# Performance work log

Hardware: AMD Instinct MI355X
Metric: run time of the kernel (lower is better)

Reference implementation:

```python
import jax, jax.numpy as jnp
import numpy as np

N = 50000          # nodes
E = 1000000        # edges
EMB = 64           # emb_dim
L = 3              # num_layer
B = 250            # graphs (200 nodes each)
XF, EF = 7, 5      # node / edge feature dims
BN_EPS = 1e-5


def setup_inputs() -> dict:
    key = jax.random.key(0)
    ks = jax.random.split(key, 16)
    x = jax.random.normal(ks[0], (N, XF), dtype=jnp.float32)
    edge_attr = jax.random.normal(ks[1], (E, EF), dtype=jnp.float32)
    edge_index = jax.random.randint(ks[2], (2, E), 0, N, dtype=jnp.int32)
    # 250 contiguous graphs of 200 nodes: last node index of each graph
    last_idx = jnp.arange(1, B + 1, dtype=jnp.int32) * (N // B) - 1
    s = 0.05
    xW = jax.random.normal(ks[3], (XF, EMB), dtype=jnp.float32) * s
    xb = jnp.zeros((EMB,), dtype=jnp.float32)
    eW = jax.random.normal(ks[4], (L, EF, EMB), dtype=jnp.float32) * s
    eb = jnp.zeros((L, EMB), dtype=jnp.float32)
    W1 = jax.random.normal(ks[5], (L, EMB, 2 * EMB), dtype=jnp.float32) * s
    b1 = jnp.zeros((L, 2 * EMB), dtype=jnp.float32)
    W2 = jax.random.normal(ks[6], (L, 2 * EMB, EMB), dtype=jnp.float32) * s
    b2 = jnp.zeros((L, EMB), dtype=jnp.float32)
    gamma = jnp.ones((L, EMB), dtype=jnp.float32)
    beta = jnp.zeros((L, EMB), dtype=jnp.float32)
    return {"x": x, "edge_attr": edge_attr, "edge_index": edge_index,
            "last_idx": last_idx, "xW": xW, "xb": xb, "eW": eW, "eb": eb,
            "W1": W1, "b1": b1, "W2": W2, "b2": b2,
            "gamma": gamma, "beta": beta}


def _gnn_forward(x, edge_attr, edge_index, last_idx, xW, xb, eW, eb, W1, b1, W2, b2, gamma, beta):
    n = x.shape[0]
    # self-loop edge attrs: first column = 8, rest 0
    self_attr = jnp.zeros((n, EF), dtype=edge_attr.dtype).at[:, 0].set(8.0)
    ea = jnp.concatenate([edge_attr, self_attr], axis=0)          # [E+N, EF]
    loop = jnp.arange(n, dtype=edge_index.dtype)
    src = jnp.concatenate([edge_index[0], loop])                  # x_j indices
    dst = jnp.concatenate([edge_index[1], loop])                  # aggregation targets

    h = x @ xW + xb                                               # [N, EMB]
    for l in range(L):
        e = ea @ eW[l] + eb[l]                                    # [E+N, EMB]
        msg = h[src] + e                                          # gather + combine
        agg = jax.ops.segment_sum(msg, dst, num_segments=n)       # scatter-add
        h2 = jax.nn.relu(agg @ W1[l] + b1[l]) @ W2[l] + b2[l]     # GIN MLP
        mean = jnp.mean(h2, axis=0)
        var = jnp.mean(jnp.square(h2 - mean), axis=0)             # biased, like torch BN
        hn = (h2 - mean) * jax.lax.rsqrt(var + BN_EPS) * gamma[l] + beta[l]
        h = jax.nn.elu(hn) if l < L - 1 else hn                   # drop_ratio = 0
    return h[last_idx]                                            # super-node reps [B, EMB]


def reference(x, edge_attr, edge_index, last_idx, xW, xb, eW, eb, W1, b1, W2, b2, gamma, beta):
    return _gnn_forward(x, edge_attr, edge_index, last_idx, xW, xb, eW, eb, W1, b1, W2, b2, gamma, beta)
```

## Files before the change

### kernel.cpp

```cpp
#include <hip/hip_runtime.h>

#define N_NODES 50000
#define N_EDGES 1000000
#define EMB     64
#define HID     128
#define NLAYER  3
#define NGRAPH  250
#define XFD     7
#define EFD     5
#define BN_EPS  1e-5f

#define BKT_SH 8
#define BKT_SZ 256
#define NBKT   ((N_NODES + BKT_SZ - 1) / BKT_SZ)
#define CHKE   4096
#define NCHK   ((N_EDGES + CHKE - 1) / CHKE)
#define CNTM   (NBKT * NCHK)
#define NB2    ((CNTM + 255) / 256)

typedef short bf8_t __attribute__((ext_vector_type(8)));
typedef float f4_t  __attribute__((ext_vector_type(4)));

union FragU {
    uint4 q;
    bf8_t v;
    unsigned short u[8];
};

__device__ __forceinline__ void atomAddF(float* p, float v) {
    __hip_atomic_fetch_add(p, v, __ATOMIC_RELAXED, __HIP_MEMORY_SCOPE_AGENT);
}

__device__ __forceinline__ unsigned short f2bf(float f) {
    unsigned int u = __float_as_uint(f);
    u += 0x7fffu + ((u >> 16) & 1u);
    return (unsigned short)(u >> 16);
}
__device__ __forceinline__ float bf2f(unsigned short s) {
    return __uint_as_float(((unsigned int)s) << 16);
}
__device__ __forceinline__ float4 bf4(ushort4 u) {
    return make_float4(bf2f(u.x), bf2f(u.y), bf2f(u.z), bf2f(u.w));
}

__global__ void k_input(const float* __restrict__ x, const float* __restrict__ xW,
                        const float* __restrict__ xb, unsigned short* __restrict__ h) {
    int gid = blockIdx.x * 256 + threadIdx.x;
    if (gid >= N_NODES * EMB) return;
    int n = gid >> 6, f = gid & 63;
    float acc = xb[f];
#pragma unroll
    for (int k = 0; k < XFD; ++k) acc = fmaf(x[n * XFD + k], xW[k * EMB + f], acc);
    h[gid] = f2bf(acc);
}

__global__ void k_packW(const float* __restrict__ W1, const float* __restrict__ W2,
                        unsigned short* __restrict__ pw1, unsigned short* __restrict__ pw2) {
    int gid = blockIdx.x * 256 + threadIdx.x;
    int layer = gid >> 14;
    int r = gid & 16383;
    if (layer >= NLAYER) return;
    if (r < 8192) {
        int p = r;
        int j = p & 7, lane = (p >> 3) & 63, ts = p >> 9;
        int t = ts >> 1, s = ts & 1;
        int k = 32 * s + 8 * (lane >> 4) + j;
        int n = 16 * t + (lane & 15);
        pw1[layer * 8192 + p] = f2bf(W1[layer * EMB * HID + k * HID + n]);
    } else {
        int p = r - 8192;
        int j = p & 7, lane = (p >> 3) & 63, ts = p >> 9;
        int t = ts >> 2, s = ts & 3;
        int k = 32 * s + 8 * (lane >> 4) + j;
        int n = 16 * t + (lane & 15);
        pw2[layer * 8192 + p] = f2bf(W2[layer * HID * EMB + k * EMB + n]);
    }
}

__global__ __launch_bounds__(256) void k_binA(const int* __restrict__ dst,
                                              int* __restrict__ cntmat) {
    __shared__ int hist[NBKT];
    int tid = threadIdx.x, c = blockIdx.x;
    for (int i = tid; i < NBKT; i += 256) hist[i] = 0;
    __syncthreads();
    int e0 = c * CHKE, e1 = min(e0 + CHKE, N_EDGES);
    for (int i = e0 + tid; i < e1; i += 256) atomicAdd(&hist[dst[i] >> BKT_SH], 1);
    __syncthreads();
    for (int b = tid; b < NBKT; b += 256) cntmat[b * NCHK + c] = hist[b];
}

__global__ __launch_bounds__(256) void k_gscanA(const int* __restrict__ in, int n,
                                                int* __restrict__ bsum) {
    int tid = threadIdx.x, lane = tid & 63, wid = tid >> 6;
    int i = blockIdx.x * 256 + tid;
    int v = (i < n) ? in[i] : 0;
#pragma unroll
    for (int off = 32; off; off >>= 1) v += __shfl_down(v, off);
    __shared__ int ws[4];
    if (lane == 0) ws[wid] = v;
    __syncthreads();
    if (tid == 0) bsum[blockIdx.x] = ws[0] + ws[1] + ws[2] + ws[3];
}

__global__ __launch_bounds__(256) void k_gscanB(const int* __restrict__ bsum, int nb,
                                                int* __restrict__ boff) {
    int tid = threadIdx.x, lane = tid & 63, wid = tid >> 6;
    int v = (tid < nb) ? bsum[tid] : 0;
    int x = v;
#pragma unroll
    for (int off = 1; off < 64; off <<= 1) {
        int y = __shfl_up(x, off);
        if (lane >= off) x += y;
    }
    __shared__ int wtot[4];
    if (lane == 63) wtot[wid] = x;
    __syncthreads();
    int woff = 0;
    for (int w = 0; w < wid; ++w) woff += wtot[w];
    if (tid < nb) boff[tid] = woff + x - v;
}

__global__ __launch_bounds__(256) void k_gscanC(const int* __restrict__ in, int n,
                                                const int* __restrict__ boff,
                                                int* __restrict__ out) {
    int tid = threadIdx.x, lane = tid & 63, wid = tid >> 6;
    int i = blockIdx.x * 256 + tid;
    int v = (i < n) ? in[i] : 0;
    int x = v;
#pragma unroll
    for (int off = 1; off < 64; off <<= 1) {
        int y = __shfl_up(x, off);
        if (lane >= off) x += y;
    }
    __shared__ int wtot[4];
    if (lane == 63) wtot[wid] = x;
    __syncthreads();
    int woff = boff[blockIdx.x];
    for (int w = 0; w < wid; ++w) woff += wtot[w];
    if (i < n) out[i] = woff + x - v;
}

__global__ __launch_bounds__(256) void k_binC(const int* __restrict__ src,
                                              const int* __restrict__ dst,
                                              const int* __restrict__ off2,
                                              int2* __restrict__ bufSD) {
    __shared__ int cur[NBKT];
    int tid = threadIdx.x, c = blockIdx.x;
    for (int b = tid; b < NBKT; b += 256) cur[b] = off2[b * NCHK + c];
    __syncthreads();
    int e0 = c * CHKE, e1 = min(e0 + CHKE, N_EDGES);
    for (int i = e0 + tid; i < e1; i += 256) {
        int d = dst[i];
        int b = d >> BKT_SH;
        int p = atomicAdd(&cur[b], 1);
        bufSD[p] = make_int2(src[i], ((d & (BKT_SZ - 1)) << 20) | i);
    }
}

__global__ __launch_bounds__(256) void k_binD(const int2* __restrict__ bufSD,
                                              const int* __restrict__ off2,
                                              int* __restrict__ csr,
                                              int* __restrict__ csrE,
                                              int* __restrict__ rowstart) {
    __shared__ int hist[BKT_SZ];
    __shared__ int cur[BKT_SZ];
    __shared__ int wtot[4];
    int tid = threadIdx.x, b = blockIdx.x;
    int bstart = off2[b * NCHK];
    int bend = (b + 1 < NBKT) ? off2[(b + 1) * NCHK] : N_EDGES;
    hist[tid] = 0;
    __syncthreads();
    for (int j = bstart + tid; j < bend; j += 256)
        atomicAdd(&hist[bufSD[j].y >> 20], 1);
    __syncthreads();
    int lane = tid & 63, wid = tid >> 6;
    int v = hist[tid], x = v;
#pragma unroll
    for (int off = 1; off < 64; off <<= 1) {
        int y = __shfl_up(x, off);
        if (lane >= off) x += y;
    }
    if (lane == 63) wtot[wid] = x;
    __syncthreads();
    int woff = 0;
    for (int w = 0; w < wid; ++w) woff += wtot[w];
    int ex = woff + x - v;
    cur[tid] = ex;
    int node = b * BKT_SZ + tid;
    if (node < N_NODES) rowstart[node] = bstart + ex;
    if (b == NBKT - 1 && tid == 0) rowstart[N_NODES] = N_EDGES;
    __syncthreads();
    for (int j = bstart + tid; j < bend; j += 256) {
        int2 t = bufSD[j];
        int local = t.y >> 20;
        int p = atomicAdd(&cur[local], 1);
        csr[bstart + p] = t.x;
        csrE[bstart + p] = t.y & 0xFFFFF;
    }
}

__global__ __launch_bounds__(256) void k_aggE(const int* __restrict__ rowstart,
                                              const int* __restrict__ csrE,
                                              const float* __restrict__ ea,
                                              float* __restrict__ aggE) {
    int wid = (blockIdx.x * 256 + threadIdx.x) >> 6;
    int lane = threadIdx.x & 63;
    if (wid >= N_NODES) return;
    int j0 = rowstart[wid], j1 = rowstart[wid + 1];
    float s0 = 0.f, s1 = 0.f, s2 = 0.f, s3 = 0.f, s4 = 0.f;
    for (int j = j0 + lane; j < j1; j += 64) {
        int e = csrE[j];
        const float* p = ea + (size_t)e * EFD;
        s0 += p[0]; s1 += p[1]; s2 += p[2]; s3 += p[3]; s4 += p[4];
    }
#pragma unroll
    for (int off = 32; off; off >>= 1) {
        s0 += __shfl_down(s0, off);
        s1 += __shfl_down(s1, off);
        s2 += __shfl_down(s2, off);
        s3 += __shfl_down(s3, off);
        s4 += __shfl_down(s4, off);
    }
    if (lane == 0) {
        float* o = aggE + (size_t)wid * EFD;
        o[0] = s0; o[1] = s1; o[2] = s2; o[3] = s3; o[4] = s4;
    }
}

__global__ __launch_bounds__(256) void k_agg(const unsigned short* __restrict__ h,
                                             float* __restrict__ agg,
                                             const int* __restrict__ rowstart,
                                             const int* __restrict__ csr,
                                             const float* __restrict__ aggE,
                                             const float* __restrict__ eWl,
                                             const float* __restrict__ ebl) {
    int wave = (blockIdx.x * 256 + threadIdx.x) >> 6;
    int lane = threadIdx.x & 63;
    int nbase = wave * 4;
    if (nbase >= N_NODES) return;
    int lg = lane >> 4, lq = lane & 15;
    const ushort4* hb = (const ushort4*)h;
    const float4* eW4 = (const float4*)eWl;
    float4 ew0 = eW4[lq], ew1 = eW4[16 + lq], ew2 = eW4[32 + lq],
           ew3 = eW4[48 + lq], ew4 = eW4[64 + lq];
    float4 eb4 = ((const float4*)ebl)[lq];
    int nend = min(nbase + 4, N_NODES);
    for (int n = nbase; n < nend; ++n) {
        int j0 = rowstart[n], j1 = rowstart[n + 1];
        float4 acc = make_float4(0.f, 0.f, 0.f, 0.f);
        int j = j0;
        while (j < j1) {
            int take = j1 - j;
            if (take > 64) take = 64;
            int myid = (lane < take) ? csr[j + lane] : 0;
            int nt = (take + 3) >> 2;
            int t = 0;
            for (; t + 4 <= nt; t += 4) {
                int e0 = t * 4 + lg, e1 = e0 + 4, e2 = e0 + 8, e3 = e0 + 12;
                int s0 = __shfl(myid, e0), s1 = __shfl(myid, e1),
                    s2 = __shfl(myid, e2), s3 = __shfl(myid, e3);
                float4 v0 = bf4(hb[(size_t)s0 * 16 + lq]);
                float4 v1 = bf4(hb[(size_t)s1 * 16 + lq]);
                float4 v2 = bf4(hb[(size_t)s2 * 16 + lq]);
                float4 v3 = bf4(hb[(size_t)s3 * 16 + lq]);
                if (e0 < take) { acc.x += v0.x; acc.y += v0.y; acc.z += v0.z; acc.w += v0.w; }
                if (e1 < take) { acc.x += v1.x; acc.y += v1.y; acc.z += v1.z; acc.w += v1.w; }
                if (e2 < take) { acc.x += v2.x; acc.y += v2.y; acc.z += v2.z; acc.w += v2.w; }
                if (e3 < take) { acc.x += v3.x; acc.y += v3.y; acc.z += v3.z; acc.w += v3.w; }
            }
            for (; t < nt; ++t) {
                int e = t * 4 + lg;
                int s = __shfl(myid, e);
                float4 v = bf4(hb[(size_t)s * 16 + lq]);
                if (e < take) { acc.x += v.x; acc.y += v.y; acc.z += v.z; acc.w += v.w; }
            }
            j += take;
        }
        acc.x += __shfl_xor(acc.x, 16); acc.y += __shfl_xor(acc.y, 16);
        acc.z += __shfl_xor(acc.z, 16); acc.w += __shfl_xor(acc.w, 16);
        acc.x += __shfl_xor(acc.x, 32); acc.y += __shfl_xor(acc.y, 32);
        acc.z += __shfl_xor(acc.z, 32); acc.w += __shfl_xor(acc.w, 32);
        float a0 = aggE[n * 5 + 0], a1 = aggE[n * 5 + 1], a2 = aggE[n * 5 + 2],
              a3 = aggE[n * 5 + 3], a4 = aggE[n * 5 + 4];
        float c0 = a0 + 8.f;
        float ce = (float)(j1 - j0) + 1.f;
        float4 bb = bf4(hb[(size_t)n * 16 + lq]);
        bb.x = fmaf(c0, ew0.x, bb.x); bb.y = fmaf(c0, ew0.y, bb.y);
        bb.z = fmaf(c0, ew0.z, bb.z); bb.w = fmaf(c0, ew0.w, bb.w);
        bb.x = fmaf(a1, ew1.x, bb.x); bb.y = fmaf(a1, ew1.y, bb.y);
        bb.z = fmaf(a1, ew1.z, bb.z); bb.w = fmaf(a1, ew1.w, bb.w);
        bb.x = fmaf(a2, ew2.x, bb.x); bb.y = fmaf(a2, ew2.y, bb.y);
        bb.z = fmaf(a2, ew2.z, bb.z); bb.w = fmaf(a2, ew2.w, bb.w);
        bb.x = fmaf(a3, ew3.x, bb.x); bb.y = fmaf(a3, ew3.y, bb.y);
        bb.z = fmaf(a3, ew3.z, bb.z); bb.w = fmaf(a3, ew3.w, bb.w);
        bb.x = fmaf(a4, ew4.x, bb.x); bb.y = fmaf(a4, ew4.y, bb.y);
        bb.z = fmaf(a4, ew4.z, bb.z); bb.w = fmaf(a4, ew4.w, bb.w);
        bb.x = fmaf(ce, eb4.x, bb.x); bb.y = fmaf(ce, eb4.y, bb.y);
        bb.z = fmaf(ce, eb4.z, bb.z); bb.w = fmaf(ce, eb4.w, bb.w);
        if (lg == 0) {
            ((float4*)agg)[(size_t)n * 16 + lq] =
                make_float4(acc.x + bb.x, acc.y + bb.y, acc.z + bb.z, acc.w + bb.w);
        }
    }
}

__global__ __launch_bounds__(256) void k_mlp(const float* __restrict__ agg,
                                             float* __restrict__ h2,
                                             const unsigned short* __restrict__ pw1,
                                             const float* __restrict__ b1l,
                                             const unsigned short* __restrict__ pw2,
                                             const float* __restrict__ b2l,
                                             float* __restrict__ stats) {
    __shared__ __align__(16) unsigned short hid[64 * 136];
    int tid = threadIdx.x;
    int w = tid >> 6, lane = tid & 63;
    int q = lane >> 4, l15 = lane & 15;
    int n0 = blockIdx.x * 64;
    int mrow = n0 + 16 * w + l15;
    const float* arow = agg + (size_t)(mrow < N_NODES ? mrow : N_NODES - 1) * EMB;
    FragU fa[2];
#pragma unroll
    for (int s = 0; s < 2; ++s) {
        float4 x0 = *(const float4*)&arow[32 * s + 8 * q];
        float4 x1 = *(const float4*)&arow[32 * s + 8 * q + 4];
        fa[s].u[0] = f2bf(x0.x); fa[s].u[1] = f2bf(x0.y);
        fa[s].u[2] = f2bf(x0.z); fa[s].u[3] = f2bf(x0.w);
        fa[s].u[4] = f2bf(x1.x); fa[s].u[5] = f2bf(x1.y);
        fa[s].u[6] = f2bf(x1.z); fa[s].u[7] = f2bf(x1.w);
    }
    const uint4* w1f = (const uint4*)pw1;
    f4_t acc1[8];
#pragma unroll
    for (int t = 0; t < 8; ++t) {
        acc1[t] = (f4_t){0.f, 0.f, 0.f, 0.f};
        FragU b0, b1;
        b0.q = w1f[(t * 2 + 0) * 64 + lane];
        b1.q = w1f[(t * 2 + 1) * 64 + lane];
        acc1[t] = __builtin_amdgcn_mfma_f32_16x16x32_bf16(fa[0].v, b0.v, acc1[t], 0, 0, 0);
        acc1[t] = __builtin_amdgcn_mfma_f32_16x16x32_bf16(fa[1].v, b1.v, acc1[t], 0, 0, 0);
    }
#pragma unroll
    for (int t = 0; t < 8; ++t) {
        int col = 16 * t + l15;
        float bv = b1l[col];
#pragma unroll
        for (int r = 0; r < 4; ++r) {
            int m = 16 * w + q * 4 + r;
            hid[m * 136 + col] = f2bf(fmaxf(acc1[t][r] + bv, 0.f));
        }
    }
    FragU fa2[4];
#pragma unroll
    for (int s = 0; s < 4; ++s)
        fa2[s].q = *(const uint4*)&hid[(16 * w + l15) * 136 + 32 * s + 8 * q];
    const uint4* w2f = (const uint4*)pw2;
    f4_t acc2[4];
#pragma unroll
    for (int t = 0; t < 4; ++t) {
        acc2[t] = (f4_t){0.f, 0.f, 0.f, 0.f};
#pragma unroll
        for (int s = 0; s < 4; ++s) {
            FragU b;
            b.q = w2f[(t * 4 + s) * 64 + lane];
            acc2[t] = __builtin_amdgcn_mfma_f32_16x16x32_bf16(fa2[s].v, b.v, acc2[t], 0, 0, 0);
        }
    }
    float sacc[4] = {0.f, 0.f, 0.f, 0.f}, qacc[4] = {0.f, 0.f, 0.f, 0.f};
#pragma unroll
    for (int t = 0; t < 4; ++t) {
        int col = 16 * t + l15;
        float bv = b2l[col];
#pragma unroll
        for (int r = 0; r < 4; ++r) {
            int nn = n0 + 16 * w + q * 4 + r;
            if (nn < N_NODES) {
                float v = acc2[t][r] + bv;
                h2[(size_t)nn * EMB + col] = v;
                sacc[t] += v;
                qacc[t] = fmaf(v, v, qacc[t]);
            }
        }
    }
#pragma unroll
    for (int t = 0; t < 4; ++t) {
        sacc[t] += __shfl_xor(sacc[t], 16); qacc[t] += __shfl_xor(qacc[t], 16);
        sacc[t] += __shfl_xor(sacc[t], 32); qacc[t] += __shfl_xor(qacc[t], 32);
    }
    __syncthreads();
    float* red = (float*)hid;
    if (q == 0) {
#pragma unroll
        for (int t = 0; t < 4; ++t) {
            red[w * 64 + 16 * t + l15] = sacc[t];
            red[256 + w * 64 + 16 * t + l15] = qacc[t];
        }
    }
    __syncthreads();
    if (tid < 64) {
        float s = red[tid] + red[64 + tid] + red[128 + tid] + red[192 + tid];
        float qq = red[256 + tid] + red[320 + tid] + red[384 + tid] + red[448 + tid];
        atomAddF(&stats[tid], s);
        atomAddF(&stats[64 + tid], qq);
    }
}

__global__ void k_bn(const float* __restrict__ h2, unsigned short* __restrict__ h,
                     const float* __restrict__ stats, const float* __restrict__ gam,
                     const float* __restrict__ bet) {
    int gid = blockIdx.x * 256 + threadIdx.x;
    if (gid >= N_NODES * EMB) return;
    int f = gid & 63;
    const float invN = 1.f / (float)N_NODES;
    float mean = stats[f] * invN;
    float var = stats[64 + f] * invN - mean * mean;
    float inv = rsqrtf(var + BN_EPS);
    float v = (h2[gid] - mean) * inv * gam[f] + bet[f];
    h[gid] = f2bf(v > 0.f ? v : expm1f(v));
}

__global__ void k_bnout(const float* __restrict__ h2, const int* __restrict__ last,
                        const float* __restrict__ stats, const float* __restrict__ gam,
                        const float* __restrict__ bet, float* __restrict__ out) {
    int gid = blockIdx.x * 256 + threadIdx.x;
    if (gid >= NGRAPH * EMB) return;
    int b = gid >> 6, f = gid & 63;
    const float invN = 1.f / (float)N_NODES;
    float mean = stats[f] * invN;
    float var = stats[64 + f] * invN - mean * mean;
    float inv = rsqrtf(var + BN_EPS);
    out[gid] = (h2[last[b] * EMB + f] - mean) * inv * gam[f] + bet[f];
}

extern "C" void kernel_launch(void* const* d_in, const int* in_sizes, int n_in,
                              void* d_out, int out_size, void* d_ws, size_t ws_size,
                              hipStream_t stream) {
    const float* x   = (const float*)d_in[0];
    const float* ea  = (const float*)d_in[1];
    const int*   eidx= (const int*)d_in[2];
    const int*   last= (const int*)d_in[3];
    const float* xW  = (const float*)d_in[4];
    const float* xb  = (const float*)d_in[5];
    const float* eW  = (const float*)d_in[6];
    const float* eb  = (const float*)d_in[7];
    const float* W1  = (const float*)d_in[8];
    const float* b1  = (const float*)d_in[9];
    const float* W2  = (const float*)d_in[10];
    const float* b2  = (const float*)d_in[11];
    const float* gam = (const float*)d_in[12];
    const float* bet = (const float*)d_in[13];
    float* out = (float*)d_out;

    const int* srcI = eidx;
    const int* dstI = eidx + N_EDGES;

    float* hslot  = (float*)d_ws;
    float* agg    = hslot + N_NODES * EMB;
    float* hidslot= agg + N_NODES * EMB;
    float* aggE   = hidslot + N_NODES * HID;
    float* stats  = aggE + NBKT * BKT_SZ * EFD;
    int* rowstart = (int*)(stats + NLAYER * 2 * EMB);
    int* csr      = rowstart + N_NODES + 1;
    int* cntmat   = csr + N_EDGES;
    int* off2     = cntmat + CNTM;
    int* bsum     = off2 + CNTM;
    int* boff     = bsum + NB2;
    unsigned short* pw1 = (unsigned short*)(boff + NB2);
    unsigned short* pw2 = pw1 + NLAYER * EMB * HID;
    unsigned short* h = (unsigned short*)hslot;
    int2* bufSD   = (int2*)agg;
    int*  csrE    = (int*)hidslot;

    hipMemsetAsync(stats, 0, NLAYER * 2 * EMB * sizeof(float), stream);

    k_input<<<(N_NODES * EMB + 255) / 256, 256, 0, stream>>>(x, xW, xb, h);
    k_packW<<<(NLAYER * 2 * EMB * HID + 255) / 256, 256, 0, stream>>>(W1, W2, pw1, pw2);
    k_binA<<<NCHK, 256, 0, stream>>>(dstI, cntmat);
    k_gscanA<<<NB2, 256, 0, stream>>>(cntmat, CNTM, bsum);
    k_gscanB<<<1, 256, 0, stream>>>(bsum, NB2, boff);
    k_gscanC<<<NB2, 256, 0, stream>>>(cntmat, CNTM, boff, off2);
    k_binC<<<NCHK, 256, 0, stream>>>(srcI, dstI, off2, bufSD);
    k_binD<<<NBKT, 256, 0, stream>>>(bufSD, off2, csr, csrE, rowstart);
    k_aggE<<<(N_NODES * 64 + 255) / 256, 256, 0, stream>>>(rowstart, csrE, ea, aggE);

    const int aggBlocks = ((N_NODES + 3) / 4 * 64 + 255) / 256;
    const int mlpBlocks = (N_NODES + 63) / 64;
    for (int l = 0; l < NLAYER; ++l) {
        k_agg<<<aggBlocks, 256, 0, stream>>>(
            h, agg, rowstart, csr, aggE, eW + l * EFD * EMB, eb + l * EMB);
        k_mlp<<<mlpBlocks, 256, 0, stream>>>(agg, agg, pw1 + l * EMB * HID, b1 + l * HID,
                                             pw2 + l * HID * EMB, b2 + l * EMB,
                                             stats + l * 2 * EMB);
        if (l < NLAYER - 1) {
            k_bn<<<(N_NODES * EMB + 255) / 256, 256, 0, stream>>>(
                agg, h, stats + l * 2 * EMB, gam + l * EMB, bet + l * EMB);
        } else {
            k_bnout<<<(NGRAPH * EMB + 255) / 256, 256, 0, stream>>>(
                agg, last, stats + l * 2 * EMB, gam + l * EMB, bet + l * EMB, out);
        }
    }
}
```

Measured before the change: 347.2 us.

## Fuse edge-attribute aggregation into binning and widen neighbor gather loads

New measurement: 361.6 us. 1.04x slower.

```diff
diff --git a/kernel.cpp b/kernel.cpp
--- a/kernel.cpp
+++ b/kernel.cpp
@@ -30,6 +30,9 @@
 __device__ __forceinline__ void atomAddF(float* p, float v) {
     __hip_atomic_fetch_add(p, v, __ATOMIC_RELAXED, __HIP_MEMORY_SCOPE_AGENT);
 }
+__device__ __forceinline__ void atomAddLDS(float* p, float v) {
+    __hip_atomic_fetch_add(p, v, __ATOMIC_RELAXED, __HIP_MEMORY_SCOPE_WORKGROUP);
+}
 
 __device__ __forceinline__ unsigned short f2bf(float f) {
     unsigned int u = __float_as_uint(f);
@@ -46,8 +49,9 @@
 __global__ void k_input(const float* __restrict__ x, const float* __restrict__ xW,
                         const float* __restrict__ xb, unsigned short* __restrict__ h) {
     int gid = blockIdx.x * 256 + threadIdx.x;
-    if (gid >= N_NODES * EMB) return;
+    if (gid >= (N_NODES + 1) * EMB) return;
     int n = gid >> 6, f = gid & 63;
+    if (n == N_NODES) { h[gid] = 0; return; }
     float acc = xb[f];
 #pragma unroll
     for (int k = 0; k < XFD; ++k) acc = fmaf(x[n * XFD + k], xW[k * EMB + f], acc);
@@ -159,16 +163,20 @@
 
 __global__ __launch_bounds__(256) void k_binD(const int2* __restrict__ bufSD,
                                               const int* __restrict__ off2,
+                                              const float* __restrict__ ea,
                                               int* __restrict__ csr,
-                                              int* __restrict__ csrE,
-                                              int* __restrict__ rowstart) {
+                                              int* __restrict__ rowstart,
+                                              float* __restrict__ aggE) {
     __shared__ int hist[BKT_SZ];
     __shared__ int cur[BKT_SZ];
     __shared__ int wtot[4];
+    __shared__ float lagg[EFD][BKT_SZ];
     int tid = threadIdx.x, b = blockIdx.x;
     int bstart = off2[b * NCHK];
     int bend = (b + 1 < NBKT) ? off2[(b + 1) * NCHK] : N_EDGES;
     hist[tid] = 0;
+#pragma unroll
+    for (int c = 0; c < EFD; ++c) lagg[c][tid] = 0.f;
     __syncthreads();
     for (int j = bstart + tid; j < bend; j += 256)
         atomicAdd(&hist[bufSD[j].y >> 20], 1);
@@ -193,39 +201,36 @@
     for (int j = bstart + tid; j < bend; j += 256) {
         int2 t = bufSD[j];
         int local = t.y >> 20;
+        int eid = t.y & 0xFFFFF;
         int p = atomicAdd(&cur[local], 1);
         csr[bstart + p] = t.x;
-        csrE[bstart + p] = t.y & 0xFFFFF;
-    }
-}
-
-__global__ __launch_bounds__(256) void k_aggE(const int* __restrict__ rowstart,
-                                              const int* __restrict__ csrE,
-                                              const float* __restrict__ ea,
-                                              float* __restrict__ aggE) {
-    int wid = (blockIdx.x * 256 + threadIdx.x) >> 6;
-    int lane = threadIdx.x & 63;
-    if (wid >= N_NODES) return;
-    int j0 = rowstart[wid], j1 = rowstart[wid + 1];
-    float s0 = 0.f, s1 = 0.f, s2 = 0.f, s3 = 0.f, s4 = 0.f;
-    for (int j = j0 + lane; j < j1; j += 64) {
-        int e = csrE[j];
-        const float* p = ea + (size_t)e * EFD;
-        s0 += p[0]; s1 += p[1]; s2 += p[2]; s3 += p[3]; s4 += p[4];
-    }
-#pragma unroll
-    for (int off = 32; off; off >>= 1) {
-        s0 += __shfl_down(s0, off);
-        s1 += __shfl_down(s1, off);
-        s2 += __shfl_down(s2, off);
-        s3 += __shfl_down(s3, off);
-        s4 += __shfl_down(s4, off);
-    }
-    if (lane == 0) {
-        float* o = aggE + (size_t)wid * EFD;
-        o[0] = s0; o[1] = s1; o[2] = s2; o[3] = s3; o[4] = s4;
-    }
-}
+        const float* pe = ea + (size_t)eid * EFD;
+        float e0 = pe[0], e1 = pe[1], e2 = pe[2], e3 = pe[3], e4 = pe[4];
+        atomAddLDS(&lagg[0][local], e0);
+        atomAddLDS(&lagg[1][local], e1);
+        atomAddLDS(&lagg[2][local], e2);
+        atomAddLDS(&lagg[3][local], e3);
+        atomAddLDS(&lagg[4][local], e4);
+    }
+    __syncthreads();
+    if (node < N_NODES) {
+        float* o = aggE + (size_t)node * EFD;
+#pragma unroll
+        for (int c = 0; c < EFD; ++c) o[c] = lagg[c][tid];
+    }
+}
+
+#define ACC8(v)                                                         \
+    do {                                                                \
+        f0 += __uint_as_float((v).x << 16);                             \
+        f1 += __uint_as_float((v).x & 0xffff0000u);                     \
+        f2 += __uint_as_float((v).y << 16);                             \
+        f3 += __uint_as_float((v).y & 0xffff0000u);                     \
+        f4 += __uint_as_float((v).z << 16);                             \
+        f5 += __uint_as_float((v).z & 0xffff0000u);                     \
+        f6 += __uint_as_float((v).w << 16);                             \
+        f7 += __uint_as_float((v).w & 0xffff0000u);                     \
+    } while (0)
 
 __global__ __launch_bounds__(256) void k_agg(const unsigned short* __restrict__ h,
                                              float* __restrict__ agg,
@@ -238,8 +243,10 @@
     int lane = threadIdx.x & 63;
     int nbase = wave * 4;
     if (nbase >= N_NODES) return;
+    int lg3 = lane >> 3, lq3 = lane & 7;
     int lg = lane >> 4, lq = lane & 15;
-    const ushort4* hb = (const ushort4*)h;
+    const uint4* hb8 = (const uint4*)h;
+    const ushort4* hb4 = (const ushort4*)h;
     const float4* eW4 = (const float4*)eWl;
     float4 ew0 = eW4[lq], ew1 = eW4[16 + lq], ew2 = eW4[32 + lq],
            ew3 = eW4[48 + lq], ew4 = eW4[64 + lq];
@@ -247,44 +254,56 @@
     int nend = min(nbase + 4, N_NODES);
     for (int n = nbase; n < nend; ++n) {
         int j0 = rowstart[n], j1 = rowstart[n + 1];
-        float4 acc = make_float4(0.f, 0.f, 0.f, 0.f);
-        int j = j0;
-        while (j < j1) {
+        float f0 = 0.f, f1 = 0.f, f2 = 0.f, f3 = 0.f,
+              f4 = 0.f, f5 = 0.f, f6 = 0.f, f7 = 0.f;
+        for (int j = j0; j < j1;) {
             int take = j1 - j;
             if (take > 64) take = 64;
-            int myid = (lane < take) ? csr[j + lane] : 0;
-            int nt = (take + 3) >> 2;
-            int t = 0;
-            for (; t + 4 <= nt; t += 4) {
-                int e0 = t * 4 + lg, e1 = e0 + 4, e2 = e0 + 8, e3 = e0 + 12;
-                int s0 = __shfl(myid, e0), s1 = __shfl(myid, e1),
-                    s2 = __shfl(myid, e2), s3 = __shfl(myid, e3);
-                float4 v0 = bf4(hb[(size_t)s0 * 16 + lq]);
-                float4 v1 = bf4(hb[(size_t)s1 * 16 + lq]);
-                float4 v2 = bf4(hb[(size_t)s2 * 16 + lq]);
-                float4 v3 = bf4(hb[(size_t)s3 * 16 + lq]);
-                if (e0 < take) { acc.x += v0.x; acc.y += v0.y; acc.z += v0.z; acc.w += v0.w; }
-                if (e1 < take) { acc.x += v1.x; acc.y += v1.y; acc.z += v1.z; acc.w += v1.w; }
-                if (e2 < take) { acc.x += v2.x; acc.y += v2.y; acc.z += v2.z; acc.w += v2.w; }
-                if (e3 < take) { acc.x += v3.x; acc.y += v3.y; acc.z += v3.z; acc.w += v3.w; }
-            }
-            for (; t < nt; ++t) {
-                int e = t * 4 + lg;
-                int s = __shfl(myid, e);
-                float4 v = bf4(hb[(size_t)s * 16 + lq]);
-                if (e < take) { acc.x += v.x; acc.y += v.y; acc.z += v.z; acc.w += v.w; }
+            int myid = (lane < take) ? csr[j + lane] : N_NODES;
+            int s0 = __shfl(myid, lg3);
+            int s1 = __shfl(myid, 8 + lg3);
+            int s2 = __shfl(myid, 16 + lg3);
+            int s3 = __shfl(myid, 24 + lg3);
+            uint4 v0 = hb8[(size_t)s0 * 8 + lq3];
+            uint4 v1 = hb8[(size_t)s1 * 8 + lq3];
+            uint4 v2 = hb8[(size_t)s2 * 8 + lq3];
+            uint4 v3 = hb8[(size_t)s3 * 8 + lq3];
+            ACC8(v0); ACC8(v1); ACC8(v2); ACC8(v3);
+            if (take > 32) {
+                int s4 = __shfl(myid, 32 + lg3);
+                int s5 = __shfl(myid, 40 + lg3);
+                int s6 = __shfl(myid, 48 + lg3);
+                int s7 = __shfl(myid, 56 + lg3);
+                uint4 w0 = hb8[(size_t)s4 * 8 + lq3];
+                uint4 w1 = hb8[(size_t)s5 * 8 + lq3];
+                uint4 w2 = hb8[(size_t)s6 * 8 + lq3];
+                uint4 w3 = hb8[(size_t)s7 * 8 + lq3];
+                ACC8(w0); ACC8(w1); ACC8(w2); ACC8(w3);
             }
             j += take;
         }
-        acc.x += __shfl_xor(acc.x, 16); acc.y += __shfl_xor(acc.y, 16);
-        acc.z += __shfl_xor(acc.z, 16); acc.w += __shfl_xor(acc.w, 16);
-        acc.x += __shfl_xor(acc.x, 32); acc.y += __shfl_xor(acc.y, 32);
-        acc.z += __shfl_xor(acc.z, 32); acc.w += __shfl_xor(acc.w, 32);
+#define RED8(F)                     \
+        F += __shfl_xor(F, 8);      \
+        F += __shfl_xor(F, 16);     \
+        F += __shfl_xor(F, 32);
+        RED8(f0) RED8(f1) RED8(f2) RED8(f3) RED8(f4) RED8(f5) RED8(f6) RED8(f7)
+#undef RED8
+        int srcl = lq >> 1;
+        float x0 = __shfl(f0, srcl), x4 = __shfl(f4, srcl);
+        float x1 = __shfl(f1, srcl), x5 = __shfl(f5, srcl);
+        float x2 = __shfl(f2, srcl), x6 = __shfl(f6, srcl);
+        float x3 = __shfl(f3, srcl), x7 = __shfl(f7, srcl);
+        bool hiHalf = (lq & 1) != 0;
+        float4 acc;
+        acc.x = hiHalf ? x4 : x0;
+        acc.y = hiHalf ? x5 : x1;
+        acc.z = hiHalf ? x6 : x2;
+        acc.w = hiHalf ? x7 : x3;
         float a0 = aggE[n * 5 + 0], a1 = aggE[n * 5 + 1], a2 = aggE[n * 5 + 2],
               a3 = aggE[n * 5 + 3], a4 = aggE[n * 5 + 4];
         float c0 = a0 + 8.f;
         float ce = (float)(j1 - j0) + 1.f;
-        float4 bb = bf4(hb[(size_t)n * 16 + lq]);
+        float4 bb = bf4(hb4[(size_t)n * 16 + lq]);
         bb.x = fmaf(c0, ew0.x, bb.x); bb.y = fmaf(c0, ew0.y, bb.y);
         bb.z = fmaf(c0, ew0.z, bb.z); bb.w = fmaf(c0, ew0.w, bb.w);
         bb.x = fmaf(a1, ew1.x, bb.x); bb.y = fmaf(a1, ew1.y, bb.y);
@@ -303,6 +322,7 @@
         }
     }
 }
+#undef ACC8
 
 __global__ __launch_bounds__(256) void k_mlp(const float* __restrict__ agg,
                                              float* __restrict__ h2,
@@ -454,9 +474,8 @@
     const int* dstI = eidx + N_EDGES;
 
     float* hslot  = (float*)d_ws;
-    float* agg    = hslot + N_NODES * EMB;
-    float* hidslot= agg + N_NODES * EMB;
-    float* aggE   = hidslot + N_NODES * HID;
+    float* agg    = hslot + (N_NODES + 1) * EMB;
+    float* aggE   = agg + N_NODES * EMB;
     float* stats  = aggE + NBKT * BKT_SZ * EFD;
     int* rowstart = (int*)(stats + NLAYER * 2 * EMB);
     int* csr      = rowstart + N_NODES + 1;
@@ -468,19 +487,17 @@
     unsigned short* pw2 = pw1 + NLAYER * EMB * HID;
     unsigned short* h = (unsigned short*)hslot;
     int2* bufSD   = (int2*)agg;
-    int*  csrE    = (int*)hidslot;
 
     hipMemsetAsync(stats, 0, NLAYER * 2 * EMB * sizeof(float), stream);
 
-    k_input<<<(N_NODES * EMB + 255) / 256, 256, 0, stream>>>(x, xW, xb, h);
+    k_input<<<((N_NODES + 1) * EMB + 255) / 256, 256, 0, stream>>>(x, xW, xb, h);
     k_packW<<<(NLAYER * 2 * EMB * HID + 255) / 256, 256, 0, stream>>>(W1, W2, pw1, pw2);
     k_binA<<<NCHK, 256, 0, stream>>>(dstI, cntmat);
     k_gscanA<<<NB2, 256, 0, stream>>>(cntmat, CNTM, bsum);
     k_gscanB<<<1, 256, 0, stream>>>(bsum, NB2, boff);
     k_gscanC<<<NB2, 256, 0, stream>>>(cntmat, CNTM, boff, off2);
     k_binC<<<NCHK, 256, 0, stream>>>(srcI, dstI, off2, bufSD);
-    k_binD<<<NBKT, 256, 0, stream>>>(bufSD, off2, csr, csrE, rowstart);
-    k_aggE<<<(N_NODES * 64 + 255) / 256, 256, 0, stream>>>(rowstart, csrE, ea, aggE);
+    k_binD<<<NBKT, 256, 0, stream>>>(bufSD, off2, ea, csr, rowstart, aggE);
 
     const int aggBlocks = ((N_NODES + 3) / 4 * 64 + 255) / 256;
     const int mlpBlocks = (N_NODES + 63) / 64;
```
